# Optimization experiments

Measured on AMD Instinct MI355X. Metric: run time of the kernel, lower is better.

## Reference

```python
import jax, jax.numpy as jnp
import numpy as np

N_SRC, N_DST = 20000, 20000
N = N_SRC + N_DST            # homogeneous node count
E = 320000                   # bipartite edges
H, D, IN = 8, 16, 128        # heads, per-head dim, input dim
TEM = 0.7
NEG_SLOPE = 0.2              # DGL GATConv leaky_relu slope
E_NEG = E - int(round(E * 0.01))  # drop-edge keeps 316800 edges


def setup_inputs() -> dict:
    key = jax.random.key(0)
    ks = jax.random.split(key, 6)
    feat = jax.random.normal(ks[0], (N, IN), jnp.float32)
    edge_src = jax.random.randint(ks[1], (E,), 0, N_SRC, dtype=jnp.int32)
    edge_dst = jax.random.randint(ks[2], (E,), 0, N_DST, dtype=jnp.int32) + N_SRC
    rng = np.random.default_rng(0)
    neg_idx = jnp.asarray(np.sort(rng.permutation(E)[:E_NEG]).astype(np.int32))
    fc_w = jax.random.normal(ks[3], (IN, H * D), jnp.float32) / np.sqrt(IN).astype(np.float32)
    attn_l = jax.random.normal(ks[4], (H, D), jnp.float32) * 0.1
    attn_r = jax.random.normal(ks[5], (H, D), jnp.float32) * 0.1
    bias = jnp.zeros((H * D,), jnp.float32)
    prelu_a = jnp.full((1,), 0.25, jnp.float32)
    return dict(feat=feat, fc_w=fc_w, attn_l=attn_l, attn_r=attn_r, bias=bias,
                prelu_a=prelu_a, edge_src=edge_src, edge_dst=edge_dst, neg_idx=neg_idx)


def _gat(feat, fc_w, attn_l, attn_r, bias, prelu_a, src, dst):
    """DGL GATConv (attn_drop=0, bias=True, activation=PReLU) + self-loops, then head-mean."""
    loop = jnp.arange(N, dtype=src.dtype)
    src = jnp.concatenate([src, loop])
    dst = jnp.concatenate([dst, loop])
    z = (feat @ fc_w).reshape(N, H, D)                 # [N,H,D]
    el = jnp.sum(z * attn_l[None], axis=-1)            # [N,H]
    er = jnp.sum(z * attn_r[None], axis=-1)            # [N,H]
    e = el[src] + er[dst]                              # [E',H]
    e = jnp.where(e >= 0, e, NEG_SLOPE * e)            # leaky_relu
    # segment (edge) softmax over incoming edges of each dst node
    m = jax.ops.segment_max(e, dst, num_segments=N)
    w = jnp.exp(e - m[dst])
    denom = jax.ops.segment_sum(w, dst, num_segments=N)
    alpha = w / denom[dst]                             # [E',H]
    msg = alpha[:, :, None] * z[src]                   # [E',H,D]
    rst = jax.ops.segment_sum(msg, dst, num_segments=N)  # [N,H,D]
    rst = rst + bias.reshape(1, H, D)
    rst = jnp.where(rst >= 0, rst, prelu_a[0] * rst)   # PReLU (single param)
    return jnp.mean(rst, axis=1)                       # [N,D] head-mean


def reference(feat, fc_w, attn_l, attn_r, bias, prelu_a, edge_src, edge_dst, neg_idx):
    h = _gat(feat, fc_w, attn_l, attn_r, bias, prelu_a, edge_src, edge_dst)
    h_neg_full = _gat(feat, fc_w, attn_l, attn_r, bias, prelu_a,
                      edge_src[neg_idx], edge_dst[neg_idx])
    # predict-type (dst) nodes are ids [N_SRC, N)
    h_pos = h[N_SRC:]
    h_neg = h_neg_full[N_SRC:]
    eps = 1e-8
    num = jnp.sum(h_pos * h_neg, axis=-1)
    na = jnp.maximum(jnp.linalg.norm(h_pos, axis=-1), eps)
    nb = jnp.maximum(jnp.linalg.norm(h_neg, axis=-1), eps)
    cos = num / (na * nb)                              # F.cosine_similarity
    loss = jnp.log(jnp.sum(jnp.exp(cos / TEM)))
    return loss, h_pos
```

## Files before the change

kernel.cpp:

```cpp
#include <hip/hip_runtime.h>

#define NSRC 20000
#define NDST 20000
#define NTOT 40000
#define ETOT 320000
#define ENEG 316800
#define NH 8
#define ND 16
#define NHD 128


__global__ __launch_bounds__(256) void k_front(const float* __restrict__ A,
                                               const float* __restrict__ B,
                                               const float* __restrict__ attn_l,
                                               const float* __restrict__ attn_r,
                                               const int* __restrict__ edge_dst,
                                               const int* __restrict__ neg_idx,
                                               float* __restrict__ C,
                                               float* __restrict__ el,
                                               float* __restrict__ er,
                                               int* __restrict__ count,
                                               unsigned char* __restrict__ flag) {
    const int tid = threadIdx.x;
    const int bx = blockIdx.x, by = blockIdx.y;
    if (by >= 625) {
        int t0 = ((by - 625) * 2 + bx) * 256 + tid;
        for (int i = t0; i < ETOT; i += 32768)
            atomicAdd(&count[edge_dst[i] - NSRC], 1);
        for (int i = t0; i < ENEG; i += 32768) flag[neg_idx[i]] = 1;
        return;
    }
    __shared__ float As[16][64];
    __shared__ float Bs[16][64];
    const int tx = tid & 15, ty = tid >> 4;
    const int row0 = by * 64 + ty * 4;
    const int col0 = bx * 64 + tx * 4;
    const int lr = tid >> 2, ls = tid & 3;
    const int br = tid >> 4, bs = tid & 15;
    float acc[4][4] = {};
    for (int k0 = 0; k0 < 128; k0 += 16) {
        float4 av = *(const float4*)(A + (by * 64 + lr) * 128 + k0 + ls * 4);
        float4 bv = *(const float4*)(B + (k0 + br) * 128 + bx * 64 + bs * 4);
        __syncthreads();
        As[ls * 4 + 0][lr] = av.x;
        As[ls * 4 + 1][lr] = av.y;
        As[ls * 4 + 2][lr] = av.z;
        As[ls * 4 + 3][lr] = av.w;
        *(float4*)(&Bs[br][bs * 4]) = bv;
        __syncthreads();
#pragma unroll
        for (int k = 0; k < 16; ++k) {
            float4 a = *(const float4*)(&As[k][ty * 4]);
            float4 b = *(const float4*)(&Bs[k][tx * 4]);
            acc[0][0] = fmaf(a.x, b.x, acc[0][0]);
            acc[0][1] = fmaf(a.x, b.y, acc[0][1]);
            acc[0][2] = fmaf(a.x, b.z, acc[0][2]);
            acc[0][3] = fmaf(a.x, b.w, acc[0][3]);
            acc[1][0] = fmaf(a.y, b.x, acc[1][0]);
            acc[1][1] = fmaf(a.y, b.y, acc[1][1]);
            acc[1][2] = fmaf(a.y, b.z, acc[1][2]);
            acc[1][3] = fmaf(a.y, b.w, acc[1][3]);
            acc[2][0] = fmaf(a.z, b.x, acc[2][0]);
            acc[2][1] = fmaf(a.z, b.y, acc[2][1]);
            acc[2][2] = fmaf(a.z, b.z, acc[2][2]);
            acc[2][3] = fmaf(a.z, b.w, acc[2][3]);
            acc[3][0] = fmaf(a.w, b.x, acc[3][0]);
            acc[3][1] = fmaf(a.w, b.y, acc[3][1]);
            acc[3][2] = fmaf(a.w, b.z, acc[3][2]);
            acc[3][3] = fmaf(a.w, b.w, acc[3][3]);
        }
    }
#pragma unroll
    for (int i = 0; i < 4; ++i) {
        *(float4*)(C + (row0 + i) * 128 + col0) =
            make_float4(acc[i][0], acc[i][1], acc[i][2], acc[i][3]);
    }
    const int hh = bx * 4 + (tx >> 2);
    const int q = tx & 3;
    float4 lv = *(const float4*)(attn_l + hh * ND + q * 4);
    float4 rv = *(const float4*)(attn_r + hh * ND + q * 4);
    float pl[4], pr[4];
#pragma unroll
    for (int i = 0; i < 4; ++i) {
        pl[i] = acc[i][0] * lv.x + acc[i][1] * lv.y + acc[i][2] * lv.z + acc[i][3] * lv.w;
        pr[i] = acc[i][0] * rv.x + acc[i][1] * rv.y + acc[i][2] * rv.z + acc[i][3] * rv.w;
    }
#pragma unroll
    for (int s = 1; s <= 2; s <<= 1) {
#pragma unroll
        for (int i = 0; i < 4; ++i) {
            pl[i] += __shfl_xor(pl[i], s, 64);
            pr[i] += __shfl_xor(pr[i], s, 64);
        }
    }
    if (q == 0) {
#pragma unroll
        for (int i = 0; i < 4; ++i) {
            el[(row0 + i) * NH + hh] = pl[i];
            er[(row0 + i) * NH + hh] = pr[i];
        }
    }
}

__global__ __launch_bounds__(1024) void k_scan(const int* __restrict__ count,
                                               int* __restrict__ rowstart) {
    __shared__ int wsum[16];
    const int tid = threadIdx.x;
    const int lane = tid & 63, w = tid >> 6;
    const int base = tid * 20;
    int c[20];
    int s = 0;
#pragma unroll
    for (int k = 0; k < 20; ++k) {
        int i = base + k;
        int v = (i < NDST) ? count[i] : 0;
        c[k] = s;
        s += v;
    }
    int v = s;
    for (int sh = 1; sh < 64; sh <<= 1) {
        int t = __shfl_up(v, sh, 64);
        if (lane >= sh) v += t;
    }
    if (lane == 63) wsum[w] = v;
    __syncthreads();
    int carry = 0;
    for (int ww = 0; ww < w; ++ww) carry += wsum[ww];
    int excl = carry + v - s;
#pragma unroll
    for (int k = 0; k < 20; ++k) {
        int i = base + k;
        if (i < NDST) rowstart[i] = excl + c[k];
    }
    if (tid == 1023) rowstart[NDST] = carry + v;
}

__global__ __launch_bounds__(256) void k_scatter(const int* __restrict__ edge_src,
                                                 const int* __restrict__ edge_dst,
                                                 const unsigned char* __restrict__ flag,
                                                 const int* __restrict__ rowstart,
                                                 int* __restrict__ cursor,
                                                 int* __restrict__ csr) {
    int i = blockIdx.x * 256 + threadIdx.x;
    if (i >= ETOT) return;
    int d = edge_dst[i] - NSRC;
    int pos = rowstart[d] + atomicAdd(&cursor[d], 1);
    int v = edge_src[i];
    if (flag[i]) v |= (int)0x80000000u;
    csr[pos] = v;
}

__global__ __launch_bounds__(256) void k_agg(const int* __restrict__ rowstart,
                                             const int* __restrict__ csr,
                                             const float* __restrict__ z,
                                             const float* __restrict__ el,
                                             const float* __restrict__ er,
                                             const float* __restrict__ bias,
                                             const float* __restrict__ prelu_a,
                                             float* __restrict__ out,
                                             float* __restrict__ expcos) {
    const int lane = threadIdx.x & 63;
    const int wid = threadIdx.x >> 6;
    const int d = (blockIdx.x << 2) + wid;

    const int g = NSRC + d;
    const int hl = lane >> 3;
    const int j8 = lane & 7;
    const float erd = er[g * NH + hl];
    const float aslope = prelu_a[0];
    const float NEGINF = -__builtin_inff();

    float mF = NEGINF, lF = 0.f, mN = NEGINF, lN = 0.f;
    float aF0 = 0.f, aF1 = 0.f, aN0 = 0.f, aN1 = 0.f;
    const int rs = rowstart[d];
    const int deg = rowstart[d + 1] - rs;

    for (int base = 0; base < deg; base += 16) {
        const int j0 = base + j8, j1 = base + 8 + j8;
        int ent0 = (j0 < deg) ? csr[rs + j0] : g;
        int ent1 = (j1 < deg) ? csr[rs + j1] : g;
        float2 zr[16];
#pragma unroll
        for (int jj = 0; jj < 16; ++jj) {
            int entry = __shfl((jj < 8) ? ent0 : ent1, jj & 7, 64);
            const float* zp = z + (size_t)(entry & 0x7FFFFFFF) * NHD + 2 * lane;
            zr[jj] = *(const float2*)zp;
        }
        float e0 = el[(size_t)(ent0 & 0x7FFFFFFF) * NH + hl] + erd;
        float e1 = el[(size_t)(ent1 & 0x7FFFFFFF) * NH + hl] + erd;
        e0 = (e0 >= 0.f) ? e0 : 0.2f * e0;
        e1 = (e1 >= 0.f) ? e1 : 0.2f * e1;
        float ev0 = (j0 < deg) ? e0 : NEGINF;
        float ev1 = (j1 < deg) ? e1 : NEGINF;
        const int fl0 = (j0 < deg) && (ent0 < 0);
        const int fl1 = (j1 < deg) && (ent1 < 0);
        float cmF = fmaxf(ev0, ev1);
        float cmN = fmaxf(fl0 ? ev0 : NEGINF, fl1 ? ev1 : NEGINF);
#pragma unroll
        for (int s = 1; s <= 4; s <<= 1) {
            cmF = fmaxf(cmF, __shfl_xor(cmF, s, 64));
            cmN = fmaxf(cmN, __shfl_xor(cmN, s, 64));
        }
        float nmF = fmaxf(mF, cmF);
        float scF = (nmF == mF) ? 1.f : __expf(mF - nmF);
        mF = nmF;
        float nmN = fmaxf(mN, cmN);
        float scN = (nmN == mN) ? 1.f : __expf(mN - nmN);
        mN = nmN;
        float wf0 = __expf(ev0 - mF);
        float wf1 = __expf(ev1 - mF);
        float wn0 = fl0 ? __expf(ev0 - mN) : 0.f;
        float wn1 = fl1 ? __expf(ev1 - mN) : 0.f;
        lF = lF * scF + wf0 + wf1;
        lN = lN * scN + wn0 + wn1;
        float w0 = fl0 ? -wf0 : wf0;
        float w1 = fl1 ? -wf1 : wf1;
        float sNh = __expf(mF - mN);
        aF0 *= scF; aF1 *= scF; aN0 *= scN; aN1 *= scN;
#pragma unroll
        for (int jj = 0; jj < 16; ++jj) {
            float v = __shfl((jj < 8) ? w0 : w1, (lane & 56) | (jj & 7), 64);
            float wf = fabsf(v);
            float wn = (v < 0.f) ? wf * sNh : 0.f;
            aF0 = fmaf(wf, zr[jj].x, aF0);
            aF1 = fmaf(wf, zr[jj].y, aF1);
            aN0 = fmaf(wn, zr[jj].x, aN0);
            aN1 = fmaf(wn, zr[jj].y, aN1);
        }
    }

    {
        float e = el[g * NH + hl] + erd;
        e = (e >= 0.f) ? e : 0.2f * e;
        float nmF = fmaxf(mF, e);
        float scF = (nmF == mF) ? 1.f : __expf(mF - nmF);
        lF *= scF; aF0 *= scF; aF1 *= scF; mF = nmF;
        float wf = __expf(e - mF);
        float nmN = fmaxf(mN, e);
        float scN = (nmN == mN) ? 1.f : __expf(mN - nmN);
        lN *= scN; aN0 *= scN; aN1 *= scN; mN = nmN;
        float wn = __expf(e - mN);
        if (j8 == 0) { lF += wf; lN += wn; }
        float2 zv = *(const float2*)(z + (size_t)g * NHD + 2 * lane);
        aF0 = fmaf(wf, zv.x, aF0);
        aF1 = fmaf(wf, zv.y, aF1);
        aN0 = fmaf(wn, zv.x, aN0);
        aN1 = fmaf(wn, zv.y, aN1);
    }

#pragma unroll
    for (int s = 1; s <= 4; s <<= 1) {
        lF += __shfl_xor(lF, s, 64);
        lN += __shfl_xor(lN, s, 64);
    }
    const int c0 = 2 * lane;
    float b0 = bias[c0], b1 = bias[c0 + 1];
    float rF0 = aF0 / lF + b0, rF1 = aF1 / lF + b1;
    float rN0 = aN0 / lN + b0, rN1 = aN1 / lN + b1;
    rF0 = (rF0 >= 0.f) ? rF0 : aslope * rF0;
    rF1 = (rF1 >= 0.f) ? rF1 : aslope * rF1;
    rN0 = (rN0 >= 0.f) ? rN0 : aslope * rN0;
    rN1 = (rN1 >= 0.f) ? rN1 : aslope * rN1;
#pragma unroll
    for (int s = 8; s <= 32; s <<= 1) {
        rF0 += __shfl_xor(rF0, s, 64);
        rF1 += __shfl_xor(rF1, s, 64);
        rN0 += __shfl_xor(rN0, s, 64);
        rN1 += __shfl_xor(rN1, s, 64);
    }
    float hF0 = rF0 * 0.125f, hF1 = rF1 * 0.125f;
    float hN0 = rN0 * 0.125f, hN1 = rN1 * 0.125f;
    if (lane < 8) {
        out[1 + d * ND + 2 * lane] = hF0;
        out[1 + d * ND + 2 * lane + 1] = hF1;
    }
    float num = hF0 * hN0 + hF1 * hN1;
    float na = hF0 * hF0 + hF1 * hF1;
    float nb = hN0 * hN0 + hN1 * hN1;
#pragma unroll
    for (int s = 1; s <= 4; s <<= 1) {
        num += __shfl_xor(num, s, 64);
        na += __shfl_xor(na, s, 64);
        nb += __shfl_xor(nb, s, 64);
    }
    if (lane == 0) {
        float cosv = num / (fmaxf(sqrtf(na), 1e-8f) * fmaxf(sqrtf(nb), 1e-8f));
        expcos[d] = __expf(cosv / 0.7f);
    }
}

__global__ __launch_bounds__(1024) void k_loss(const float* __restrict__ expcos,
                                               float* __restrict__ out) {
    __shared__ float sbuf[16];
    float s = 0.f;
    for (int i = threadIdx.x; i < NDST; i += 1024) s += expcos[i];
    for (int sh = 1; sh < 64; sh <<= 1) s += __shfl_xor(s, sh, 64);
    if ((threadIdx.x & 63) == 0) sbuf[threadIdx.x >> 6] = s;
    __syncthreads();
    if (threadIdx.x < 16) {
        float t = sbuf[threadIdx.x];
        for (int sh = 1; sh < 16; sh <<= 1) t += __shfl_xor(t, sh, 16);
        if (threadIdx.x == 0) out[0] = logf(t);
    }
}

extern "C" void kernel_launch(void* const* d_in, const int* in_sizes, int n_in,
                              void* d_out, int out_size, void* d_ws, size_t ws_size,
                              hipStream_t stream) {
    const float* feat = (const float*)d_in[0];
    const float* fc_w = (const float*)d_in[1];
    const float* attn_l = (const float*)d_in[2];
    const float* attn_r = (const float*)d_in[3];
    const float* bias = (const float*)d_in[4];
    const float* prelu_a = (const float*)d_in[5];
    const int* edge_src = (const int*)d_in[6];
    const int* edge_dst = (const int*)d_in[7];
    const int* neg_idx = (const int*)d_in[8];
    float* out = (float*)d_out;

    char* ws = (char*)d_ws;
    int* count = (int*)(ws + 0);
    int* cursor = (int*)(ws + 80000);
    unsigned char* flag = (unsigned char*)(ws + 160000);
    int* rowstart = (int*)(ws + 480000);
    int* csr = (int*)(ws + 560064);
    float* expcos = (float*)(ws + 1840064);
    float* z = (float*)(ws + 1920064);
    float* el = (float*)(ws + 22400064);
    float* er = (float*)(ws + 23680064);

    hipMemsetAsync(d_ws, 0, 480000, stream);
    k_front<<<dim3(2, 689), 256, 0, stream>>>(feat, fc_w, attn_l, attn_r,
                                              edge_dst, neg_idx, z, el, er,
                                              count, flag);
    k_scan<<<1, 1024, 0, stream>>>(count, rowstart);
    k_scatter<<<(ETOT + 255) / 256, 256, 0, stream>>>(edge_src, edge_dst, flag,
                                                      rowstart, cursor, csr);
    k_agg<<<NDST / 4, 256, 0, stream>>>(rowstart, csr, z, el, er, bias, prelu_a,
                                        out, expcos);
    k_loss<<<1, 1024, 0, stream>>>(expcos, out);
}
```

Before: 176.8 us.

## Use bf16 MFMA for projection and store z in bf16 for gather

Replaces the fp32 SIMT tiled GEMM in the front kernel with bf16 MFMA 16x16x32 instructions. The full weight matrix is staged in LDS as transposed bf16, and the grid becomes 1D with 625 GEMM blocks plus 128 counting blocks. The projected features z are now stored as bf16, halving the bytes gathered per edge in the aggregation kernel, which unpacks them with bit shifts. Attention logits are still computed from the fp32 accumulators. The trade-off is reduced precision in z and in the GEMM inputs, which may affect accuracy tolerance.

```diff
diff --git a/kernel.cpp b/kernel.cpp
--- a/kernel.cpp
+++ b/kernel.cpp
@@ -8,6 +8,10 @@
 #define NH 8
 #define ND 16
 #define NHD 128
+#define BSTRIDE 136
+
+typedef __bf16 v8bf __attribute__((ext_vector_type(8)));
+typedef float v4f __attribute__((ext_vector_type(4)));
 
 
 __global__ __launch_bounds__(256) void k_front(const float* __restrict__ A,
@@ -16,88 +20,74 @@
                                                const float* __restrict__ attn_r,
                                                const int* __restrict__ edge_dst,
                                                const int* __restrict__ neg_idx,
-                                               float* __restrict__ C,
+                                               unsigned short* __restrict__ z,
                                                float* __restrict__ el,
                                                float* __restrict__ er,
                                                int* __restrict__ count,
                                                unsigned char* __restrict__ flag) {
     const int tid = threadIdx.x;
-    const int bx = blockIdx.x, by = blockIdx.y;
-    if (by >= 625) {
-        int t0 = ((by - 625) * 2 + bx) * 256 + tid;
+    const int bid = blockIdx.x;
+    if (bid >= 625) {
+        int t0 = (bid - 625) * 256 + tid;
         for (int i = t0; i < ETOT; i += 32768)
             atomicAdd(&count[edge_dst[i] - NSRC], 1);
         for (int i = t0; i < ENEG; i += 32768) flag[neg_idx[i]] = 1;
         return;
     }
-    __shared__ float As[16][64];
-    __shared__ float Bs[16][64];
-    const int tx = tid & 15, ty = tid >> 4;
-    const int row0 = by * 64 + ty * 4;
-    const int col0 = bx * 64 + tx * 4;
-    const int lr = tid >> 2, ls = tid & 3;
-    const int br = tid >> 4, bs = tid & 15;
-    float acc[4][4] = {};
-    for (int k0 = 0; k0 < 128; k0 += 16) {
-        float4 av = *(const float4*)(A + (by * 64 + lr) * 128 + k0 + ls * 4);
-        float4 bv = *(const float4*)(B + (k0 + br) * 128 + bx * 64 + bs * 4);
-        __syncthreads();
-        As[ls * 4 + 0][lr] = av.x;
-        As[ls * 4 + 1][lr] = av.y;
-        As[ls * 4 + 2][lr] = av.z;
-        As[ls * 4 + 3][lr] = av.w;
-        *(float4*)(&Bs[br][bs * 4]) = bv;
-        __syncthreads();
-#pragma unroll
-        for (int k = 0; k < 16; ++k) {
-            float4 a = *(const float4*)(&As[k][ty * 4]);
-            float4 b = *(const float4*)(&Bs[k][tx * 4]);
-            acc[0][0] = fmaf(a.x, b.x, acc[0][0]);
-            acc[0][1] = fmaf(a.x, b.y, acc[0][1]);
-            acc[0][2] = fmaf(a.x, b.z, acc[0][2]);
-            acc[0][3] = fmaf(a.x, b.w, acc[0][3]);
-            acc[1][0] = fmaf(a.y, b.x, acc[1][0]);
-            acc[1][1] = fmaf(a.y, b.y, acc[1][1]);
-            acc[1][2] = fmaf(a.y, b.z, acc[1][2]);
-            acc[1][3] = fmaf(a.y, b.w, acc[1][3]);
-            acc[2][0] = fmaf(a.z, b.x, acc[2][0]);
-            acc[2][1] = fmaf(a.z, b.y, acc[2][1]);
-            acc[2][2] = fmaf(a.z, b.z, acc[2][2]);
-            acc[2][3] = fmaf(a.z, b.w, acc[2][3]);
-            acc[3][0] = fmaf(a.w, b.x, acc[3][0]);
-            acc[3][1] = fmaf(a.w, b.y, acc[3][1]);
-            acc[3][2] = fmaf(a.w, b.z, acc[3][2]);
-            acc[3][3] = fmaf(a.w, b.w, acc[3][3]);
-        }
-    }
-#pragma unroll
-    for (int i = 0; i < 4; ++i) {
-        *(float4*)(C + (row0 + i) * 128 + col0) =
-            make_float4(acc[i][0], acc[i][1], acc[i][2], acc[i][3]);
-    }
-    const int hh = bx * 4 + (tx >> 2);
-    const int q = tx & 3;
-    float4 lv = *(const float4*)(attn_l + hh * ND + q * 4);
-    float4 rv = *(const float4*)(attn_r + hh * ND + q * 4);
-    float pl[4], pr[4];
-#pragma unroll
-    for (int i = 0; i < 4; ++i) {
-        pl[i] = acc[i][0] * lv.x + acc[i][1] * lv.y + acc[i][2] * lv.z + acc[i][3] * lv.w;
-        pr[i] = acc[i][0] * rv.x + acc[i][1] * rv.y + acc[i][2] * rv.z + acc[i][3] * rv.w;
-    }
-#pragma unroll
-    for (int s = 1; s <= 2; s <<= 1) {
-#pragma unroll
-        for (int i = 0; i < 4; ++i) {
-            pl[i] += __shfl_xor(pl[i], s, 64);
-            pr[i] += __shfl_xor(pr[i], s, 64);
-        }
-    }
-    if (q == 0) {
-#pragma unroll
-        for (int i = 0; i < 4; ++i) {
-            el[(row0 + i) * NH + hh] = pl[i];
-            er[(row0 + i) * NH + hh] = pr[i];
+    __shared__ __bf16 Bs[128 * BSTRIDE];
+    for (int i = tid; i < 4096; i += 256) {
+        float4 v = ((const float4*)B)[i];
+        int k = (i * 4) >> 7;
+        int n = (i * 4) & 127;
+        Bs[(n + 0) * BSTRIDE + k] = (__bf16)v.x;
+        Bs[(n + 1) * BSTRIDE + k] = (__bf16)v.y;
+        Bs[(n + 2) * BSTRIDE + k] = (__bf16)v.z;
+        Bs[(n + 3) * BSTRIDE + k] = (__bf16)v.w;
+    }
+    __syncthreads();
+    const int w = tid >> 6, lane = tid & 63;
+    const int ml = lane & 15, q = lane >> 4;
+    const int gm = bid * 64 + w * 16 + ml;
+    v4f acc[8];
+#pragma unroll
+    for (int n = 0; n < 8; ++n) acc[n] = (v4f){0.f, 0.f, 0.f, 0.f};
+#pragma unroll
+    for (int ks = 0; ks < 4; ++ks) {
+        const int k0 = ks * 32 + q * 8;
+        float4 f0 = *(const float4*)(A + (size_t)gm * 128 + k0);
+        float4 f1 = *(const float4*)(A + (size_t)gm * 128 + k0 + 4);
+        v8bf av;
+        av[0] = (__bf16)f0.x; av[1] = (__bf16)f0.y;
+        av[2] = (__bf16)f0.z; av[3] = (__bf16)f0.w;
+        av[4] = (__bf16)f1.x; av[5] = (__bf16)f1.y;
+        av[6] = (__bf16)f1.z; av[7] = (__bf16)f1.w;
+#pragma unroll
+        for (int n = 0; n < 8; ++n) {
+            v8bf bv = *(const v8bf*)(&Bs[(n * 16 + ml) * BSTRIDE + k0]);
+            acc[n] = __builtin_amdgcn_mfma_f32_16x16x32_bf16(av, bv, acc[n], 0, 0, 0);
+        }
+    }
+    const int rowbase = bid * 64 + w * 16 + q * 4;
+#pragma unroll
+    for (int n = 0; n < 8; ++n) {
+        float alv = attn_l[n * 16 + ml];
+        float arv = attn_r[n * 16 + ml];
+#pragma unroll
+        for (int r = 0; r < 4; ++r) {
+            float v = acc[n][r];
+            unsigned int u = __float_as_uint(v);
+            unsigned int b = (u + 0x7fffu + ((u >> 16) & 1u)) >> 16;
+            z[(size_t)(rowbase + r) * NHD + n * 16 + ml] = (unsigned short)b;
+            float pl = v * alv, pr = v * arv;
+#pragma unroll
+            for (int s = 1; s <= 8; s <<= 1) {
+                pl += __shfl_xor(pl, s, 64);
+                pr += __shfl_xor(pr, s, 64);
+            }
+            if (ml == 0) {
+                el[(rowbase + r) * NH + n] = pl;
+                er[(rowbase + r) * NH + n] = pr;
+            }
         }
     }
 }
@@ -152,7 +142,7 @@
 
 __global__ __launch_bounds__(256) void k_agg(const int* __restrict__ rowstart,
                                              const int* __restrict__ csr,
-                                             const float* __restrict__ z,
+                                             const unsigned short* __restrict__ z,
                                              const float* __restrict__ el,
                                              const float* __restrict__ er,
                                              const float* __restrict__ bias,
@@ -179,12 +169,11 @@
         const int j0 = base + j8, j1 = base + 8 + j8;
         int ent0 = (j0 < deg) ? csr[rs + j0] : g;
         int ent1 = (j1 < deg) ? csr[rs + j1] : g;
-        float2 zr[16];
+        unsigned int zr[16];
 #pragma unroll
         for (int jj = 0; jj < 16; ++jj) {
             int entry = __shfl((jj < 8) ? ent0 : ent1, jj & 7, 64);
-            const float* zp = z + (size_t)(entry & 0x7FFFFFFF) * NHD + 2 * lane;
-            zr[jj] = *(const float2*)zp;
+            zr[jj] = *(const unsigned int*)(z + ((size_t)(entry & 0x7FFFFFFF) << 7) + 2 * lane);
         }
         float e0 = el[(size_t)(ent0 & 0x7FFFFFFF) * NH + hl] + erd;
         float e1 = el[(size_t)(ent1 & 0x7FFFFFFF) * NH + hl] + erd;
@@ -222,10 +211,12 @@
             float v = __shfl((jj < 8) ? w0 : w1, (lane & 56) | (jj & 7), 64);
             float wf = fabsf(v);
             float wn = (v < 0.f) ? wf * sNh : 0.f;
-            aF0 = fmaf(wf, zr[jj].x, aF0);
-            aF1 = fmaf(wf, zr[jj].y, aF1);
-            aN0 = fmaf(wn, zr[jj].x, aN0);
-            aN1 = fmaf(wn, zr[jj].y, aN1);
+            float zx = __uint_as_float(zr[jj] << 16);
+            float zy = __uint_as_float(zr[jj] & 0xffff0000u);
+            aF0 = fmaf(wf, zx, aF0);
+            aF1 = fmaf(wf, zy, aF1);
+            aN0 = fmaf(wn, zx, aN0);
+            aN1 = fmaf(wn, zy, aN1);
         }
     }
 
@@ -241,11 +232,13 @@
         lN *= scN; aN0 *= scN; aN1 *= scN; mN = nmN;
         float wn = __expf(e - mN);
         if (j8 == 0) { lF += wf; lN += wn; }
-        float2 zv = *(const float2*)(z + (size_t)g * NHD + 2 * lane);
-        aF0 = fmaf(wf, zv.x, aF0);
-        aF1 = fmaf(wf, zv.y, aF1);
-        aN0 = fmaf(wn, zv.x, aN0);
-        aN1 = fmaf(wn, zv.y, aN1);
+        unsigned int zv = *(const unsigned int*)(z + ((size_t)g << 7) + 2 * lane);
+        float zx = __uint_as_float(zv << 16);
+        float zy = __uint_as_float(zv & 0xffff0000u);
+        aF0 = fmaf(wf, zx, aF0);
+        aF1 = fmaf(wf, zy, aF1);
+        aN0 = fmaf(wn, zx, aN0);
+        aN1 = fmaf(wn, zy, aN1);
     }
 
 #pragma unroll
@@ -325,14 +318,13 @@
     int* rowstart = (int*)(ws + 480000);
     int* csr = (int*)(ws + 560064);
     float* expcos = (float*)(ws + 1840064);
-    float* z = (float*)(ws + 1920064);
-    float* el = (float*)(ws + 22400064);
-    float* er = (float*)(ws + 23680064);
+    unsigned short* z = (unsigned short*)(ws + 1920064);
+    float* el = (float*)(ws + 12160064);
+    float* er = (float*)(ws + 13440064);
 
     hipMemsetAsync(d_ws, 0, 480000, stream);
-    k_front<<<dim3(2, 689), 256, 0, stream>>>(feat, fc_w, attn_l, attn_r,
-                                              edge_dst, neg_idx, z, el, er,
-                                              count, flag);
+    k_front<<<753, 256, 0, stream>>>(feat, fc_w, attn_l, attn_r, edge_dst,
+                                     neg_idx, z, el, er, count, flag);
     k_scan<<<1, 1024, 0, stream>>>(count, rowstart);
     k_scatter<<<(ETOT + 255) / 256, 256, 0, stream>>>(edge_src, edge_dst, flag,
                                                       rowstart, cursor, csr);
```

Result: no change. 178.7 us (+1.0%).
